# Optimization experiments

Hardware: AMD Instinct MI355X
Metric: run time of the kernel (lower is better)

The kernel has to match this reference:

```python
import jax, jax.numpy as jnp
import numpy as np

L, B, N, D, H, DH, M = 2, 8, 1024, 256, 4, 64, 512
EPS = 1e-5


def setup_inputs() -> dict:
    key = jax.random.key(0)
    ks = jax.random.split(key, 24)
    n = lambda k, shape, s=0.02: jax.random.normal(k, shape, dtype=jnp.float32) * s
    return {
        "x": jax.random.normal(ks[0], (B, N, D), dtype=jnp.float32),
        "ln1_g": jnp.ones((L, D), jnp.float32), "ln1_b": jnp.zeros((L, D), jnp.float32),
        "w_qkv": n(ks[1], (L, D, 3 * H * DH)),
        "w_out": n(ks[2], (L, H * DH, D)), "b_out": jnp.zeros((L, D), jnp.float32),
        "ln2_g": jnp.ones((L, D), jnp.float32), "ln2_b": jnp.zeros((L, D), jnp.float32),
        "w_fc1": n(ks[3], (L, D, M)), "b_fc1": jnp.zeros((L, M), jnp.float32),
        "wh": n(ks[4], (L, M, 3), 0.3), "bh": jnp.zeros((L, M), jnp.float32),
        "wv": n(ks[5], (L, M, 3), 0.3), "bv": jnp.zeros((L, M), jnp.float32),
        "bn_g": jnp.ones((L, M), jnp.float32), "bn_b": jnp.zeros((L, M), jnp.float32),
        "bn_m": n(ks[6], (L, M), 0.1),
        "bn_v": jax.random.uniform(ks[7], (L, M), jnp.float32, 0.5, 1.5),
        "w_fc2": n(ks[8], (L, M, D)), "b_fc2": jnp.zeros((L, D), jnp.float32),
        "ls_w1": n(ks[9], (L, D, D // 4)), "ls_w2": n(ks[10], (L, D // 4, D)),
    }


def _ln(z, g, b):
    mu = z.mean(-1, keepdims=True)
    var = ((z - mu) ** 2).mean(-1, keepdims=True)
    return (z - mu) / jnp.sqrt(var + EPS) * g + b


def _lsrc(z, w1, w2):
    # SE gate: global mean over tokens -> FC -> ReLU -> FC -> sigmoid -> scale
    s = jax.nn.sigmoid(jax.nn.relu(z.mean(1) @ w1) @ w2)  # [B, D]
    return z * s[:, None, :]


def reference(x, ln1_g, ln1_b, w_qkv, w_out, b_out, ln2_g, ln2_b, w_fc1, b_fc1,
              wh, bh, wv, bv, bn_g, bn_b, bn_m, bn_v, w_fc2, b_fc2, ls_w1, ls_w2):
    scale = DH ** -0.5
    for l in range(L):
        # --- MHSA (pre-LN) ---
        h = _ln(x, ln1_g[l], ln1_b[l])
        qkv = h @ w_qkv[l]                                  # [B,N,3*H*DH]
        q, k, v = jnp.split(qkv, 3, axis=-1)
        split = lambda t: t.reshape(B, N, H, DH).transpose(0, 2, 1, 3)  # [B,H,N,DH]
        q, k, v = split(q), split(k), split(v)
        attn = jax.nn.softmax(jnp.einsum('bhid,bhjd->bhij', q, k) * scale, axis=-1)
        o = jnp.einsum('bhij,bhjd->bhid', attn, v)
        o = o.transpose(0, 2, 1, 3).reshape(B, N, H * DH)
        y = o @ w_out[l] + b_out[l]                          # dropout = identity (eval)
        x = _lsrc(x + y, ls_w1[l], ls_w2[l])
        # --- MLP with ACB depthwise conv over the token axis ---
        y = jax.nn.gelu(_ln(x, ln2_g[l], ln2_b[l]) @ w_fc1[l] + b_fc1[l], approximate=False)
        # conv_h: depthwise 1x3 conv along N (zero pad)
        yp = jnp.pad(y, ((0, 0), (1, 1), (0, 0)))
        ch = wh[l, :, 0] * yp[:, :-2] + wh[l, :, 1] * yp[:, 1:-1] + wh[l, :, 2] * yp[:, 2:] + bh[l]
        # conv_v: 3x1 depthwise conv on height-1 input with pad 1 -> only center tap
        cv = wv[l, :, 1] * y + bv[l]
        z = ch + cv
        z = (z - bn_m[l]) / jnp.sqrt(bn_v[l] + EPS) * bn_g[l] + bn_b[l]  # BN (eval)
        z = jax.nn.gelu(z, approximate=False)
        y = z @ w_fc2[l] + b_fc2[l]
        x = _lsrc(x + y, ls_w1[l], ls_w2[l])
    return x
```

## Files before the change

kernel.cpp:

```cpp
#include <hip/hip_runtime.h>
#include <hip/hip_bf16.h>
#include <math.h>

#define EPSF 1e-5f

typedef short bf16x8 __attribute__((ext_vector_type(8)));
typedef float f32x4  __attribute__((ext_vector_type(4)));

__device__ __forceinline__ float gelu_f(float z){
  return 0.5f*z*(1.0f + erff(z*0.70710678118654752f));
}
__device__ __forceinline__ unsigned short f2bf(float f){
  unsigned u = __float_as_uint(f);
  u += 0x7FFFu + ((u >> 16) & 1u);
  return (unsigned short)(u >> 16);
}
__device__ __forceinline__ float bf2f(unsigned short u){
  return __uint_as_float((unsigned)u << 16);
}
__device__ __forceinline__ void gll16(const unsigned short* g, unsigned short* l){
  __builtin_amdgcn_global_load_lds(
    (const __attribute__((address_space(1))) unsigned int*)g,
    (__attribute__((address_space(3))) unsigned int*)l, 16, 0, 0);
}

__global__ void tcast_all_k(const float* __restrict__ wqkv, const float* __restrict__ wout,
                            const float* __restrict__ wfc1, const float* __restrict__ wfc2,
                            unsigned short* __restrict__ oqkv, unsigned short* __restrict__ oout,
                            unsigned short* __restrict__ ofc1, unsigned short* __restrict__ ofc2,
                            const float* __restrict__ wh, const float* __restrict__ bh,
                            const float* __restrict__ wv, const float* __restrict__ bv,
                            const float* __restrict__ g, const float* __restrict__ bb,
                            const float* __restrict__ mm, const float* __restrict__ vv,
                            float* __restrict__ cp){
  int idx = blockIdx.x*256 + threadIdx.x;
  if (idx < 1048576){
    int l = idx >> 19; int r = idx & 524287;
    const float* in; unsigned short* out; int K, N, base;
    if (r < 196608)      { in=wqkv+ (long)l*196608; out=oqkv+(long)l*196608; K=256; N=768; base=r; }
    else if (r < 262144) { in=wout+ (long)l*65536;  out=oout+(long)l*65536;  K=256; N=256; base=r-196608; }
    else if (r < 393216) { in=wfc1+ (long)l*131072; out=ofc1+(long)l*131072; K=256; N=512; base=r-262144; }
    else                 { in=wfc2+ (long)l*131072; out=ofc2+(long)l*131072; K=512; N=256; base=r-393216; }
    int n = base / K, k = base % K;
    out[base] = f2bf(in[(long)k*N + n]);
  } else if (idx < 1048576 + 1024){
    int j2 = idx - 1048576;
    int l = j2 >> 9, j = j2 & 511;
    int o = l*512 + j;
    float sc = g[o]*rsqrtf(vv[o] + EPSF);
    float* c = cp + (long)l*6*512;
    c[0*512+j] = wh[o*3+0];
    c[1*512+j] = wh[o*3+1] + wv[o*3+1];
    c[2*512+j] = wh[o*3+2];
    c[3*512+j] = bh[o] + bv[o];
    c[4*512+j] = sc;
    c[5*512+j] = bb[o] - mm[o]*sc;
  }
}

__global__ void ln_bf_k(const float* __restrict__ x, const float* __restrict__ g,
                        const float* __restrict__ b, unsigned short* __restrict__ out){
  const int row = blockIdx.x;
  const int t = threadIdx.x;
  float v = x[(long)row*256 + t];
  float s = v, s2 = v*v;
  for (int o=32;o>0;o>>=1){ s += __shfl_down(s,o); s2 += __shfl_down(s2,o); }
  __shared__ float ls[4], ls2[4];
  const int w = t>>6, lane = t&63;
  if (lane==0){ ls[w]=s; ls2[w]=s2; }
  __syncthreads();
  if (t==0){
    float a  = ls[0]+ls[1]+ls[2]+ls[3];
    float a2 = ls2[0]+ls2[1]+ls2[2]+ls2[3];
    float mu = a*(1.f/256.f);
    float var = a2*(1.f/256.f) - mu*mu;
    ls[0]=mu; ls2[0]=rsqrtf(var+EPSF);
  }
  __syncthreads();
  out[(long)row*256+t] = f2bf((v-ls[0])*ls2[0]*g[t] + b[t]);
}

__global__ void seapply_ln_k(float* __restrict__ x, const float* __restrict__ gate,
                             const float* __restrict__ g, const float* __restrict__ b,
                             unsigned short* __restrict__ out){
  const int row = blockIdx.x;
  const int t = threadIdx.x;
  const int bi = row >> 10;
  float v = x[(long)row*256 + t] * gate[bi*256 + t];
  x[(long)row*256 + t] = v;
  float s = v, s2 = v*v;
  for (int o=32;o>0;o>>=1){ s += __shfl_down(s,o); s2 += __shfl_down(s2,o); }
  __shared__ float ls[4], ls2[4];
  const int w = t>>6, lane = t&63;
  if (lane==0){ ls[w]=s; ls2[w]=s2; }
  __syncthreads();
  if (t==0){
    float a  = ls[0]+ls[1]+ls[2]+ls[3];
    float a2 = ls2[0]+ls2[1]+ls2[2]+ls2[3];
    float mu = a*(1.f/256.f);
    float var = a2*(1.f/256.f) - mu*mu;
    ls[0]=mu; ls2[0]=rsqrtf(var+EPSF);
  }
  __syncthreads();
  out[(long)row*256+t] = f2bf((v-ls[0])*ls2[0]*g[t] + b[t]);
}

__global__ void seapply_out_k(const float* __restrict__ x, const float* __restrict__ gate,
                              float* __restrict__ o){
  long o4 = ((long)blockIdx.x*256 + threadIdx.x)*4;
  float4 v = *reinterpret_cast<const float4*>(x+o4);
  float4 g = *reinterpret_cast<const float4*>(gate + (((o4>>18)<<8) | (o4 & 255)));
  v.x*=g.x; v.y*=g.y; v.z*=g.z; v.w*=g.w;
  *reinterpret_cast<float4*>(o+o4) = v;
}

template<int ACT, bool RES, bool BIAS, int OUT, int BNT, bool CS>
__global__ __launch_bounds__(256,2)
void gmm_k(const unsigned short* __restrict__ A,
           const unsigned short* __restrict__ Bt,
           void* __restrict__ Cv, int ldc,
           const float* __restrict__ bias,
           const float* __restrict__ res,
           int K, unsigned short* __restrict__ vtb,
           float* __restrict__ cm)
{
  __shared__ unsigned short As[128*64];
  __shared__ unsigned short Bs[BNT*64];
  float* C = (float*)Cv;
  unsigned short* Cb = (unsigned short*)Cv;
  const int tid  = threadIdx.x;
  const int wave = tid>>6, lane = tid&63;
  constexpr int NJ = (BNT==128) ? 4 : 2;
  const int wm = (wave>>1)*64, wn = (wave&1)*(BNT/2);
  const int m0 = blockIdx.y*128, n0 = blockIdx.x*BNT;
  const int lrow = lane&15, quad = lane>>4;

  f32x4 acc[4][NJ];
  #pragma unroll
  for (int i=0;i<4;i++)
    #pragma unroll
    for (int j=0;j<NJ;j++)
      #pragma unroll
      for (int r=0;r<4;r++) acc[i][j][r]=0.f;

  for (int k0=0;k0<K;k0+=64){
    __syncthreads();
    #pragma unroll
    for (int it=0; it<4; it++){
      int idx = tid + it*256;
      int row = idx>>3, c = idx&7;
      gll16(A + (long)(m0+row)*K + k0 + c*8, &As[idx*8]);
    }
    #pragma unroll
    for (int it=0; it<BNT/32; it++){
      int idx = tid + it*256;
      int row = idx>>3, c = idx&7;
      gll16(Bt + (long)(n0+row)*K + k0 + c*8, &Bs[idx*8]);
    }
    __syncthreads();
    #pragma unroll
    for (int s=0;s<2;s++){
      bf16x8 a[4], b[NJ];
      const int ck = s*4 + quad;
      #pragma unroll
      for (int i=0;i<4;i++)
        a[i] = *reinterpret_cast<const bf16x8*>(&As[(wm+16*i+lrow)*64 + ck*8]);
      #pragma unroll
      for (int j=0;j<NJ;j++)
        b[j] = *reinterpret_cast<const bf16x8*>(&Bs[(wn+16*j+lrow)*64 + ck*8]);
      #pragma unroll
      for (int i=0;i<4;i++)
        #pragma unroll
        for (int j=0;j<NJ;j++)
          acc[i][j] = __builtin_amdgcn_mfma_f32_16x16x32_bf16(a[i], b[j], acc[i][j], 0,0,0);
    }
  }

  float csum[NJ];
  #pragma unroll
  for (int j=0;j<NJ;j++) csum[j] = 0.f;

  #pragma unroll
  for (int i=0;i<4;i++){
    const int row0 = m0 + wm + 16*i + quad*4;
    #pragma unroll
    for (int j=0;j<NJ;j++){
      const int col = n0 + wn + 16*j + lrow;
      if (OUT==2){
        if (col < 512){
          #pragma unroll
          for (int r=0;r<4;r++)
            Cb[(long)(row0+r)*512 + col] = f2bf(acc[i][j][r]);
        } else {
          ushort4 u;
          u.x = f2bf(acc[i][j][0]); u.y = f2bf(acc[i][j][1]);
          u.z = f2bf(acc[i][j][2]); u.w = f2bf(acc[i][j][3]);
          int bb = row0 >> 10, nn = row0 & 1023;
          int h = (col-512) >> 6, d = (col-512) & 63;
          *reinterpret_cast<ushort4*>(&vtb[(long)((bb*4+h)*64 + d)*1024 + nn]) = u;
        }
      } else {
        const float bv = BIAS ? bias[col] : 0.f;
        #pragma unroll
        for (int r=0;r<4;r++){
          const long off = (long)(row0+r)*ldc + col;
          float v = acc[i][j][r] + bv;
          if (RES) v += res[off];
          if (ACT==1) v = gelu_f(v);
          if (CS) csum[j] += v;
          if (OUT==1) Cb[off] = f2bf(v); else C[off] = v;
        }
      }
    }
  }
  if (CS){
    const int bb = m0 >> 10;
    #pragma unroll
    for (int j=0;j<NJ;j++)
      atomicAdd(&cm[bb*256 + n0 + wn + 16*j + lrow], csum[j]);
  }
}

__global__ __launch_bounds__(256)
void attn_k(const unsigned short* __restrict__ qkb,
            const unsigned short* __restrict__ vtb,
            float* __restrict__ op, float* __restrict__ ml){
  const int q0 = blockIdx.x * 64;
  const int bh = blockIdx.y;
  const int kz = blockIdx.z;
  const int b = bh >> 2, h = bh & 3;
  const int tid = threadIdx.x;
  const int wv = tid >> 6;
  const int lane = tid & 63;
  const int l15 = lane & 15, quad = lane >> 4;

  __shared__ unsigned short Qs[64*64];
  __shared__ unsigned short Ks[64*64];
  __shared__ unsigned short Vt[64*64];
  __shared__ unsigned short Ps[64*64];

  const long rowbase = (long)b*1024;
  const unsigned short* vsrc = vtb + (long)bh*64*1024;

  for (int f = tid; f < 512; f += 256){
    int row = f >> 3, g = f & 7;
    *reinterpret_cast<uint4*>(&Qs[row*64 + (g ^ (row&7))*8]) =
      *reinterpret_cast<const uint4*>(qkb + (rowbase + q0 + row)*512 + h*64 + g*8);
  }

  float lp[4];
  f32x4 acc[4];
  #pragma unroll
  for (int r=0;r<4;r++) lp[r] = 0.f;
  #pragma unroll
  for (int j=0;j<4;j++)
    #pragma unroll
    for (int r=0;r<4;r++) acc[j][r] = 0.f;

  const int kbeg = kz*512, kend = kbeg + 512;
  for (int k0 = kbeg; k0 < kend; k0 += 64){
    __syncthreads();
    for (int f = tid; f < 512; f += 256){
      int row = f >> 3, g = f & 7;
      *reinterpret_cast<uint4*>(&Ks[row*64 + (g ^ (row&7))*8]) =
        *reinterpret_cast<const uint4*>(qkb + (rowbase + k0 + row)*512 + 256 + h*64 + g*8);
      *reinterpret_cast<uint4*>(&Vt[row*64 + (g ^ (row&7))*8]) =
        *reinterpret_cast<const uint4*>(vsrc + (long)row*1024 + k0 + g*8);
    }
    __syncthreads();

    f32x4 s[4];
    #pragma unroll
    for (int j=0;j<4;j++)
      #pragma unroll
      for (int r=0;r<4;r++) s[j][r] = 0.f;

    #pragma unroll
    for (int half=0; half<2; half++){
      const int ck = half*4 + quad;
      const int qrow = 16*wv + l15;
      bf16x8 a = *reinterpret_cast<const bf16x8*>(&Qs[qrow*64 + (ck ^ (qrow&7))*8]);
      #pragma unroll
      for (int j=0;j<4;j++){
        int krow = 16*j + l15;
        bf16x8 bb = *reinterpret_cast<const bf16x8*>(&Ks[krow*64 + (ck ^ (krow&7))*8]);
        s[j] = __builtin_amdgcn_mfma_f32_16x16x32_bf16(a, bb, s[j], 0,0,0);
      }
    }

    #pragma unroll
    for (int r=0;r<4;r++)
      #pragma unroll
      for (int j=0;j<4;j++){
        float p = __expf(s[j][r]*0.125f);
        s[j][r] = p;
        lp[r] += p;
      }

    #pragma unroll
    for (int j=0;j<4;j++)
      #pragma unroll
      for (int r=0;r<4;r++){
        int rowq = 16*wv + quad*4 + r;
        int key = l15 + 16*j;
        Ps[rowq*64 + (((key>>3) ^ ((rowq>>2)&7)))*8 + (key&7)] = f2bf(s[j][r]);
      }

    #pragma unroll
    for (int half=0; half<2; half++){
      const int ck = half*4 + quad;
      const int prow = 16*wv + l15;
      bf16x8 a = *reinterpret_cast<const bf16x8*>(&Ps[prow*64 + (ck ^ ((prow>>2)&7))*8]);
      #pragma unroll
      for (int jj=0;jj<4;jj++){
        int drow = 16*jj + l15;
        bf16x8 bb = *reinterpret_cast<const bf16x8*>(&Vt[drow*64 + (ck ^ (drow&7))*8]);
        acc[jj] = __builtin_amdgcn_mfma_f32_16x16x32_bf16(a, bb, acc[jj], 0,0,0);
      }
    }
  }

  #pragma unroll
  for (int r=0;r<4;r++){
    float l = lp[r];
    l += __shfl_xor(l, 1); l += __shfl_xor(l, 2);
    l += __shfl_xor(l, 4); l += __shfl_xor(l, 8);
    const int rloc = q0 + 16*wv + quad*4 + r;
    const long grow = rowbase + rloc;
    #pragma unroll
    for (int jj=0;jj<4;jj++)
      op[((long)kz*8192 + grow)*256 + h*64 + 16*jj + l15] = acc[jj][r];
    if (l15 == 0)
      ml[((long)kz*32 + bh)*1024 + rloc] = l;
  }
}

__global__ void attn_merge_k(const float* __restrict__ op, const float* __restrict__ ml,
                             unsigned short* __restrict__ o, float* __restrict__ cm){
  if (blockIdx.x == 0){
    for (int i = threadIdx.x; i < 2048; i += 256) cm[i] = 0.f;
  }
  long off = ((long)blockIdx.x*256 + threadIdx.x)*4;
  int row = (int)(off >> 8);
  int col = (int)(off & 255);
  int h = col >> 6;
  int b = row >> 10, n = row & 1023;
  int bh = b*4 + h;
  float l0 = ml[(long)bh*1024 + n];
  float l1 = ml[32768 + (long)bh*1024 + n];
  float inv = 1.f / (l0 + l1);
  float4 a0 = *reinterpret_cast<const float4*>(op + off);
  float4 a1 = *reinterpret_cast<const float4*>(op + 2097152 + off);
  ushort4 u;
  u.x = f2bf((a0.x + a1.x)*inv);
  u.y = f2bf((a0.y + a1.y)*inv);
  u.z = f2bf((a0.z + a1.z)*inv);
  u.w = f2bf((a0.w + a1.w)*inv);
  *reinterpret_cast<ushort4*>(o + off) = u;
}

__global__ void segate2_k(const float* __restrict__ cm, const float* __restrict__ w1,
                          const float* __restrict__ w2, float* __restrict__ gate){
  const int b = blockIdx.x, t = threadIdx.x;
  __shared__ float sc[256], sh[64];
  sc[t] = cm[b*256+t]*(1.f/1024.f);
  __syncthreads();
  if (t < 64){
    float a=0.f;
    for (int k=0;k<256;k++) a += sc[k]*w1[k*64+t];
    sh[t] = fmaxf(a, 0.f);
  }
  __syncthreads();
  float a=0.f;
  for (int k=0;k<64;k++) a += sh[k]*w2[k*256+t];
  gate[b*256+t] = 1.f/(1.f+__expf(-a));
}

__global__ void conv_bf_k(const unsigned short* __restrict__ y, unsigned short* __restrict__ z,
                          const float* __restrict__ cp, float* __restrict__ cm)
{
  if (blockIdx.x == 0){
    for (int i = threadIdx.x; i < 2048; i += 256) cm[i] = 0.f;
  }
  const int t = threadIdx.x;
  const int rr = t >> 6;
  const int row = blockIdx.x*4 + rr;
  const int n = row & 1023;
  const int c8 = (t & 63) * 8;
  const long base = (long)row*512 + c8;

  uint4 uc = *reinterpret_cast<const uint4*>(y + base);
  uint4 um = (n>0)    ? *reinterpret_cast<const uint4*>(y + base - 512) : uint4{0,0,0,0};
  uint4 up = (n<1023) ? *reinterpret_cast<const uint4*>(y + base + 512) : uint4{0,0,0,0};
  const unsigned short* yc = reinterpret_cast<const unsigned short*>(&uc);
  const unsigned short* ym = reinterpret_cast<const unsigned short*>(&um);
  const unsigned short* yp = reinterpret_cast<const unsigned short*>(&up);

  float c0[8], c1[8], c2[8], c3[8], s5[8], b5[8];
  #pragma unroll
  for (int q=0;q<8;q+=4){
    *reinterpret_cast<float4*>(&c0[q]) = *reinterpret_cast<const float4*>(cp + 0*512 + c8 + q);
    *reinterpret_cast<float4*>(&c1[q]) = *reinterpret_cast<const float4*>(cp + 1*512 + c8 + q);
    *reinterpret_cast<float4*>(&c2[q]) = *reinterpret_cast<const float4*>(cp + 2*512 + c8 + q);
    *reinterpret_cast<float4*>(&c3[q]) = *reinterpret_cast<const float4*>(cp + 3*512 + c8 + q);
    *reinterpret_cast<float4*>(&s5[q]) = *reinterpret_cast<const float4*>(cp + 4*512 + c8 + q);
    *reinterpret_cast<float4*>(&b5[q]) = *reinterpret_cast<const float4*>(cp + 5*512 + c8 + q);
  }

  unsigned short outv[8];
  #pragma unroll
  for (int q=0;q<8;q++){
    float zz = c0[q]*bf2f(ym[q]) + c1[q]*bf2f(yc[q]) + c2[q]*bf2f(yp[q]) + c3[q];
    zz = zz*s5[q] + b5[q];
    outv[q] = f2bf(gelu_f(zz));
  }
  *reinterpret_cast<uint4*>(z + base) = *reinterpret_cast<uint4*>(outv);
}

extern "C" void kernel_launch(void* const* d_in, const int* in_sizes, int n_in,
                              void* d_out, int out_size, void* d_ws, size_t ws_size,
                              hipStream_t stream)
{
  const float* x_in  = (const float*)d_in[0];
  const float* ln1_g = (const float*)d_in[1];
  const float* ln1_b = (const float*)d_in[2];
  const float* w_qkv = (const float*)d_in[3];
  const float* w_out = (const float*)d_in[4];
  const float* b_out = (const float*)d_in[5];
  const float* ln2_g = (const float*)d_in[6];
  const float* ln2_b = (const float*)d_in[7];
  const float* w_fc1 = (const float*)d_in[8];
  const float* b_fc1 = (const float*)d_in[9];
  const float* wh    = (const float*)d_in[10];
  const float* bh    = (const float*)d_in[11];
  const float* wv    = (const float*)d_in[12];
  const float* bv    = (const float*)d_in[13];
  const float* bn_g  = (const float*)d_in[14];
  const float* bn_b  = (const float*)d_in[15];
  const float* bn_m  = (const float*)d_in[16];
  const float* bn_v  = (const float*)d_in[17];
  const float* w_fc2 = (const float*)d_in[18];
  const float* b_fc2 = (const float*)d_in[19];
  const float* ls_w1 = (const float*)d_in[20];
  const float* ls_w2 = (const float*)d_in[21];

  float* ws   = (float*)d_ws;
  float* xbuf = ws;
  float* opart= xbuf + 2097152;
  float* mlb  = opart + 4194304;
  float* cm   = mlb + 65536;
  float* gate = cm + 2048;
  float* cpar = gate + 2048;
  unsigned short* habf = (unsigned short*)(cpar + 6144);
  unsigned short* qkb  = habf + 2097152;
  unsigned short* vtb  = qkb  + 4194304;
  unsigned short* ybf  = vtb  + 2097152;
  unsigned short* zbf  = ybf  + 4194304;
  unsigned short* wqkv_t = zbf + 4194304;
  unsigned short* wout_t = wqkv_t + 393216;
  unsigned short* wfc1_t = wout_t + 131072;
  unsigned short* wfc2_t = wfc1_t + 262144;

  tcast_all_k<<<4100,256,0,stream>>>(w_qkv, w_out, w_fc1, w_fc2,
                                     wqkv_t, wout_t, wfc1_t, wfc2_t,
                                     wh, bh, wv, bv, bn_g, bn_b, bn_m, bn_v, cpar);

  for (int l=0;l<2;l++){
    const float* bout_l = b_out + l*256;
    const float* bfc1_l = b_fc1 + l*512;
    const float* bfc2_l = b_fc2 + l*256;
    const float* lw1_l  = ls_w1 + (long)l*256*64;
    const float* lw2_l  = ls_w2 + (long)l*64*256;
    const float* resx   = (l==0) ? x_in : xbuf;

    if (l==0)
      ln_bf_k<<<8192,256,0,stream>>>(x_in, ln1_g, ln1_b, habf);
    gmm_k<0,false,false,2,128,false><<<dim3(6,64),256,0,stream>>>(
        habf, wqkv_t + (long)l*768*256, (void*)qkb, 512, nullptr, nullptr, 256, vtb, nullptr);
    attn_k<<<dim3(16,32,2),256,0,stream>>>(qkb, vtb, opart, mlb);
    attn_merge_k<<<2048,256,0,stream>>>(opart, mlb, habf, cm);
    gmm_k<0,true,true,0,64,true><<<dim3(4,64),256,0,stream>>>(
        habf, wout_t + (long)l*256*256, (void*)xbuf, 256, bout_l, resx, 256, nullptr, cm);

    segate2_k<<<8,256,0,stream>>>(cm, lw1_l, lw2_l, gate);
    seapply_ln_k<<<8192,256,0,stream>>>(xbuf, gate, ln2_g + l*256, ln2_b + l*256, habf);

    gmm_k<1,false,true,1,128,false><<<dim3(4,64),256,0,stream>>>(
        habf, wfc1_t + (long)l*512*256, (void*)ybf, 512, bfc1_l, nullptr, 256, nullptr, nullptr);
    conv_bf_k<<<2048,256,0,stream>>>(ybf, zbf, cpar + (long)l*6*512, cm);
    gmm_k<0,true,true,0,64,true><<<dim3(4,64),256,0,stream>>>(
        zbf, wfc2_t + (long)l*256*512, (void*)xbuf, 256, bfc2_l, xbuf, 512, nullptr, cm);

    segate2_k<<<8,256,0,stream>>>(cm, lw1_l, lw2_l, gate);
    if (l==0)
      seapply_ln_k<<<8192,256,0,stream>>>(xbuf, gate, ln1_g + 256, ln1_b + 256, habf);
    else
      seapply_out_k<<<2048,256,0,stream>>>(xbuf, gate, (float*)d_out);
  }
}
```

Before: 365.5 us.

## Double-buffer GEMM LDS tiles and pre-reduce column sums in shared memory

```diff
diff --git a/kernel.cpp b/kernel.cpp
--- a/kernel.cpp
+++ b/kernel.cpp
@@ -6,6 +6,10 @@
 
 typedef short bf16x8 __attribute__((ext_vector_type(8)));
 typedef float f32x4  __attribute__((ext_vector_type(4)));
+
+#define S_BARRIER   __asm__ volatile("s_barrier" ::: "memory")
+#define S_WAITV(n)  __asm__ volatile("s_waitcnt vmcnt(" #n ")" ::: "memory")
+#define S_WAITL0    __asm__ volatile("s_waitcnt lgkmcnt(0)" ::: "memory")
 
 __device__ __forceinline__ float gelu_f(float z){
   return 0.5f*z*(1.0f + erff(z*0.70710678118654752f));
@@ -124,8 +128,8 @@
            int K, unsigned short* __restrict__ vtb,
            float* __restrict__ cm)
 {
-  __shared__ unsigned short As[128*64];
-  __shared__ unsigned short Bs[BNT*64];
+  __shared__ unsigned short As[2][128*64];
+  __shared__ unsigned short Bs[2][BNT*64];
   float* C = (float*)Cv;
   unsigned short* Cb = (unsigned short*)Cv;
   const int tid  = threadIdx.x;
@@ -143,37 +147,53 @@
       #pragma unroll
       for (int r=0;r<4;r++) acc[i][j][r]=0.f;
 
-  for (int k0=0;k0<K;k0+=64){
-    __syncthreads();
-    #pragma unroll
-    for (int it=0; it<4; it++){
-      int idx = tid + it*256;
+  auto stage = [&](int kt, int buf){
+    const int k0 = kt<<6;
+    #pragma unroll
+    for (int it2=0; it2<4; it2++){
+      int idx = tid + it2*256;
       int row = idx>>3, c = idx&7;
-      gll16(A + (long)(m0+row)*K + k0 + c*8, &As[idx*8]);
-    }
-    #pragma unroll
-    for (int it=0; it<BNT/32; it++){
-      int idx = tid + it*256;
+      gll16(A + (long)(m0+row)*K + k0 + c*8, &As[buf][idx*8]);
+    }
+    #pragma unroll
+    for (int it2=0; it2<BNT/32; it2++){
+      int idx = tid + it2*256;
       int row = idx>>3, c = idx&7;
-      gll16(Bt + (long)(n0+row)*K + k0 + c*8, &Bs[idx*8]);
-    }
-    __syncthreads();
+      gll16(Bt + (long)(n0+row)*K + k0 + c*8, &Bs[buf][idx*8]);
+    }
+  };
+
+  const int iters = K >> 6;
+  stage(0, 0);
+
+  for (int it=0; it<iters; it++){
+    const int cur = it & 1;
+    if (it+1 < iters){
+      stage(it+1, cur^1);
+      if (BNT==128) { S_WAITV(8); } else { S_WAITV(6); }
+    } else {
+      S_WAITV(0);
+    }
+    S_BARRIER;
+
     #pragma unroll
     for (int s=0;s<2;s++){
       bf16x8 a[4], b[NJ];
       const int ck = s*4 + quad;
       #pragma unroll
       for (int i=0;i<4;i++)
-        a[i] = *reinterpret_cast<const bf16x8*>(&As[(wm+16*i+lrow)*64 + ck*8]);
+        a[i] = *reinterpret_cast<const bf16x8*>(&As[cur][(wm+16*i+lrow)*64 + ck*8]);
       #pragma unroll
       for (int j=0;j<NJ;j++)
-        b[j] = *reinterpret_cast<const bf16x8*>(&Bs[(wn+16*j+lrow)*64 + ck*8]);
+        b[j] = *reinterpret_cast<const bf16x8*>(&Bs[cur][(wn+16*j+lrow)*64 + ck*8]);
       #pragma unroll
       for (int i=0;i<4;i++)
         #pragma unroll
         for (int j=0;j<NJ;j++)
           acc[i][j] = __builtin_amdgcn_mfma_f32_16x16x32_bf16(a[i], b[j], acc[i][j], 0,0,0);
     }
+    S_WAITL0;
+    S_BARRIER;
   }
 
   float csum[NJ];
@@ -214,10 +234,16 @@
     }
   }
   if (CS){
+    float* red = (float*)&As[0][0];
+    for (int j = tid; j < BNT; j += 256) red[j] = 0.f;
+    __syncthreads();
+    #pragma unroll
+    for (int j=0;j<NJ;j++)
+      atomicAdd(&red[wn + 16*j + lrow], csum[j]);
+    __syncthreads();
     const int bb = m0 >> 10;
-    #pragma unroll
-    for (int j=0;j<NJ;j++)
-      atomicAdd(&cm[bb*256 + n0 + wn + 16*j + lrow], csum[j]);
+    for (int j = tid; j < BNT; j += 256)
+      atomicAdd(&cm[bb*256 + n0 + j], red[j]);
   }
 }
 
```

Measured after the change: 346.2 us. 5.3% less time.
